# Kernel tuning notes

Measured on AMD Instinct MI355X. Metric: run time of the kernel, lower is better.

Reference implementation:

```python
import jax, jax.numpy as jnp
import numpy as np

NH = 12   # num_heads
EPS = 1e-6


def _layer_norm(x):
    m = jnp.mean(x, axis=-1, keepdims=True)
    v = jnp.mean((x - m) ** 2, axis=-1, keepdims=True)
    return (x - m) * jax.lax.rsqrt(v + EPS)


def _rms_norm(x, w):
    return x * jax.lax.rsqrt(jnp.mean(x * x, axis=-1, keepdims=True) + EPS) * w


def _rope_cos_sin(f, h, w, head_dim):
    # matches rope_params + calculate_freqs_i: split c=head_dim//2 complex freqs
    # into [c-2*(c//3), c//3, c//3] for the (F,H,W) axes.
    c = head_dim // 2
    inv = 1.0 / (10000.0 ** (np.arange(0, head_dim, 2, dtype=np.float64) / head_dim))
    c1 = c - 2 * (c // 3); c2 = c // 3
    af = np.outer(np.arange(f), inv[:c1])
    ah = np.outer(np.arange(h), inv[c1:c1 + c2])
    aw = np.outer(np.arange(w), inv[c1 + c2:])
    ang = np.concatenate([
        np.broadcast_to(af[:, None, None, :], (f, h, w, c1)),
        np.broadcast_to(ah[None, :, None, :], (f, h, w, c2)),
        np.broadcast_to(aw[None, None, :, :], (f, h, w, c2)),
    ], axis=-1).reshape(f * h * w, c)
    return jnp.asarray(np.cos(ang), jnp.float32), jnp.asarray(np.sin(ang), jnp.float32)


def _apply_rope(x, cos, sin):
    # complex rotation on interleaved pairs; x: [B,L,n,d]
    B, L, n, d = x.shape
    xr = x.reshape(B, L, n, d // 2, 2)
    x0, x1 = xr[..., 0], xr[..., 1]
    co = cos[None, :, None, :]; si = sin[None, :, None, :]
    return jnp.stack([x0 * co - x1 * si, x0 * si + x1 * co], axis=-1).reshape(B, L, n, d)


def _attention(q, k, v):
    scale = 1.0 / jnp.sqrt(jnp.asarray(q.shape[-1], q.dtype))
    s = jnp.einsum('blnd,bmnd->bnlm', q, k) * scale
    return jnp.einsum('bnlm,bmnd->blnd', jax.nn.softmax(s, axis=-1), v)


def _block(x, e, context, mod, sa_wq, sa_bq, sa_wk, sa_bk, sa_wv, sa_bv, sa_wo, sa_bo,
           sa_nq, sa_nk, n3_w, n3_b, ca_wq, ca_bq, ca_wk, ca_bk, ca_wv, ca_bv, ca_wo,
           ca_bo, ca_nq, ca_nk, ffn_w1, ffn_b1, ffn_w2, ffn_b2, f, h, w):
    B, L, C = x.shape
    D = C // NH
    em = mod + e                      # [B,6,C] AdaLN shift/scale/gate params
    cos, sin = _rope_cos_sin(f, h, w, D)
    # --- self-attention with AdaLN modulation + RoPE + qk RMSNorm ---
    xa = _layer_norm(x) * (1.0 + em[:, 1:2]) + em[:, 0:1]
    q = _rms_norm(xa @ sa_wq + sa_bq, sa_nq).reshape(B, L, NH, D)
    k = _rms_norm(xa @ sa_wk + sa_bk, sa_nk).reshape(B, L, NH, D)
    v = (xa @ sa_wv + sa_bv).reshape(B, L, NH, D)
    q = _apply_rope(q, cos, sin)
    k = _apply_rope(k, cos, sin)
    y = _attention(q, k, v).reshape(B, L, C) @ sa_wo + sa_bo
    x = x + y * em[:, 2:3]
    # --- t2v cross-attention (norm3 is affine LayerNorm) ---
    L2 = context.shape[1]
    xc = _layer_norm(x) * n3_w + n3_b
    q = _rms_norm(xc @ ca_wq + ca_bq, ca_nq).reshape(B, L, NH, D)
    k = _rms_norm(context @ ca_wk + ca_bk, ca_nk).reshape(B, L2, NH, D)
    v = (context @ ca_wv + ca_bv).reshape(B, L2, NH, D)
    x = x + (_attention(q, k, v).reshape(B, L, C) @ ca_wo + ca_bo)
    # --- FFN (GELU-tanh) with AdaLN modulation ---
    xf = _layer_norm(x) * (1.0 + em[:, 4:5]) + em[:, 3:4]
    y = jax.nn.gelu(xf @ ffn_w1 + ffn_b1, approximate=True) @ ffn_w2 + ffn_b2
    return x + y * em[:, 5:6]


def setup_inputs() -> dict:
    key = jax.random.key(0)
    ks = jax.random.split(key, 16)
    B, L2, C, FFN = 1, 512, 1536, 8960
    F, H, W = 9, 16, 28
    L = F * H * W  # 4032
    def mk(i, shape, s=0.02):
        return jax.random.normal(ks[i], shape, jnp.float32) * s
    return {
        'x': jax.random.normal(ks[0], (B, L, C), jnp.float32),
        'e': jax.random.normal(ks[1], (B, 6, C), jnp.float32),
        'context': jax.random.normal(ks[2], (B, L2, C), jnp.float32),
        'mod': jax.random.normal(ks[3], (1, 6, C), jnp.float32) / jnp.sqrt(float(C)),
        'sa_wq': mk(4, (C, C)), 'sa_bq': jnp.zeros((C,), jnp.float32),
        'sa_wk': mk(5, (C, C)), 'sa_bk': jnp.zeros((C,), jnp.float32),
        'sa_wv': mk(6, (C, C)), 'sa_bv': jnp.zeros((C,), jnp.float32),
        'sa_wo': mk(7, (C, C)), 'sa_bo': jnp.zeros((C,), jnp.float32),
        'sa_nq': jnp.ones((C,), jnp.float32), 'sa_nk': jnp.ones((C,), jnp.float32),
        'n3_w': jnp.ones((C,), jnp.float32), 'n3_b': jnp.zeros((C,), jnp.float32),
        'ca_wq': mk(8, (C, C)), 'ca_bq': jnp.zeros((C,), jnp.float32),
        'ca_wk': mk(9, (C, C)), 'ca_bk': jnp.zeros((C,), jnp.float32),
        'ca_wv': mk(10, (C, C)), 'ca_bv': jnp.zeros((C,), jnp.float32),
        'ca_wo': mk(11, (C, C)), 'ca_bo': jnp.zeros((C,), jnp.float32),
        'ca_nq': jnp.ones((C,), jnp.float32), 'ca_nk': jnp.ones((C,), jnp.float32),
        'ffn_w1': mk(12, (C, FFN)), 'ffn_b1': jnp.zeros((FFN,), jnp.float32),
        'ffn_w2': mk(13, (FFN, C)), 'ffn_b2': jnp.zeros((C,), jnp.float32),
        'f': F, 'h': H, 'w': W,
    }


def reference(x, e, context, mod, sa_wq, sa_bq, sa_wk, sa_bk, sa_wv, sa_bv, sa_wo,
              sa_bo, sa_nq, sa_nk, n3_w, n3_b, ca_wq, ca_bq, ca_wk, ca_bk, ca_wv,
              ca_bv, ca_wo, ca_bo, ca_nq, ca_nk, ffn_w1, ffn_b1, ffn_w2, ffn_b2,
              f, h, w):
    return _block(x, e, context, mod, sa_wq, sa_bq, sa_wk, sa_bk, sa_wv, sa_bv,
                  sa_wo, sa_bo, sa_nq, sa_nk, n3_w, n3_b, ca_wq, ca_bq, ca_wk,
                  ca_bk, ca_wv, ca_bv, ca_wo, ca_bo, ca_nq, ca_nk, ffn_w1, ffn_b1,
                  ffn_w2, ffn_b2, f, h, w)
```

## Files before the change

### kernel.cpp

```cpp
#include <hip/hip_runtime.h>
#include <math.h>


#define L_SEQ 4032
#define L_PAD 4096
#define C_DIM 1536
#define L_CTX 512
#define FFN_DIM 8960
#define NHEAD 12
#define DHEAD 128

typedef __attribute__((ext_vector_type(8))) short short8;
typedef __attribute__((ext_vector_type(4))) float floatx4;

__device__ inline unsigned short f2bf(float x) {
  unsigned int u = __float_as_uint(x);
  u += 0x7fffu + ((u >> 16) & 1u);
  return (unsigned short)(u >> 16);
}

__device__ inline float2 block_sum2(float2 v) {
  __shared__ float2 red[4];
#pragma unroll
  for (int o = 32; o > 0; o >>= 1) {
    v.x += __shfl_xor(v.x, o, 64);
    v.y += __shfl_xor(v.y, o, 64);
  }
  int wave = threadIdx.x >> 6;
  if ((threadIdx.x & 63) == 0) red[wave] = v;
  __syncthreads();
  float2 t = make_float2(0.f, 0.f);
#pragma unroll
  for (int i = 0; i < 4; ++i) { t.x += red[i].x; t.y += red[i].y; }
  return t;
}

__global__ void add_kernel(float* __restrict__ o, const float* __restrict__ a,
                           const float* __restrict__ b, int n) {
  int i = blockIdx.x * 256 + threadIdx.x;
  if (i < n) o[i] = a[i] + b[i];
}

__global__ void concat3_kernel(float* __restrict__ o, const float* __restrict__ a,
                               const float* __restrict__ b, const float* __restrict__ c) {
  int i = blockIdx.x * 256 + threadIdx.x;
  if (i < C_DIM) {
    o[i] = a[i];
    o[C_DIM + i] = b[i];
    if (c) o[2 * C_DIM + i] = c[i];
  }
}

__global__ void f32_to_bf16_kernel(unsigned short* __restrict__ o,
                                   const float* __restrict__ in, int n) {
  int i = (blockIdx.x * 256 + threadIdx.x) * 4;
  if (i < n) {
    float4 v = *(const float4*)&in[i];
    ushort4 o4 = {f2bf(v.x), f2bf(v.y), f2bf(v.z), f2bf(v.w)};
    *(ushort4*)&o[i] = o4;
  }
}

__global__ __launch_bounds__(256) void transpose_bf16_kernel(
    const float* __restrict__ W, unsigned short* __restrict__ WT, int K, int N) {
  __shared__ float t[32][33];
  int n0 = blockIdx.x * 32, k0 = blockIdx.y * 32;
  int c = threadIdx.x & 31, r0 = threadIdx.x >> 5;
#pragma unroll
  for (int i = 0; i < 4; ++i) {
    int r = r0 + 8 * i;
    t[r][c] = W[(size_t)(k0 + r) * N + n0 + c];
  }
  __syncthreads();
#pragma unroll
  for (int i = 0; i < 4; ++i) {
    int r = r0 + 8 * i;
    WT[(size_t)(n0 + r) * K + k0 + c] = f2bf(t[c][r]);
  }
}

__global__ __launch_bounds__(256) void transpose_v_kernel(
    const float* __restrict__ V, unsigned short* __restrict__ Vt, int stride, int Lk) {
  __shared__ float t[32][33];
  int k0 = blockIdx.x * 32, c0 = blockIdx.y * 32;
  int c = threadIdx.x & 31, r0 = threadIdx.x >> 5;
#pragma unroll
  for (int i = 0; i < 4; ++i) {
    int r = r0 + 8 * i;
    t[r][c] = V[(size_t)(k0 + r) * stride + c0 + c];
  }
  __syncthreads();
#pragma unroll
  for (int i = 0; i < 4; ++i) {
    int r = r0 + 8 * i;
    Vt[(size_t)(c0 + r) * Lk + k0 + c] = f2bf(t[c][r]);
  }
}

__global__ __launch_bounds__(256) void ln_affine_kernel(
    unsigned short* __restrict__ out, const float* __restrict__ in,
    const float* __restrict__ sc, const float* __restrict__ sh, float addOne) {
  int row = blockIdx.x;
  const float* xr = in + (size_t)row * C_DIM;
  float vals[C_DIM / 256];
  float2 p = make_float2(0.f, 0.f);
  int cnt = 0;
  for (int c = threadIdx.x; c < C_DIM; c += 256) {
    float v = xr[c];
    vals[cnt++] = v;
    p.x += v; p.y += v * v;
  }
  float2 t = block_sum2(p);
  float mean = t.x * (1.f / C_DIM);
  float var = t.y * (1.f / C_DIM) - mean * mean;
  float r = rsqrtf(var + 1e-6f);
  cnt = 0;
  for (int c = threadIdx.x; c < C_DIM; c += 256) {
    float xh = (vals[cnt++] - mean) * r;
    out[(size_t)row * C_DIM + c] = f2bf(xh * (addOne + sc[c]) + sh[c]);
  }
}

template <int ROPE>
__global__ __launch_bounds__(256) void rms_post_kernel(
    unsigned short* __restrict__ obf, const float* __restrict__ in,
    const float* __restrict__ w, const float* __restrict__ cosb,
    const float* __restrict__ sinb, int stride, float ps) {
  int row = blockIdx.x;
  const float* xr = in + (size_t)row * stride;
  int c0 = threadIdx.x * 6;
  float v[6];
  *(float2*)&v[0] = *(const float2*)&xr[c0];
  *(float2*)&v[2] = *(const float2*)&xr[c0 + 2];
  *(float2*)&v[4] = *(const float2*)&xr[c0 + 4];
  float s2 = 0.f;
#pragma unroll
  for (int i = 0; i < 6; ++i) s2 += v[i] * v[i];
  float2 t = block_sum2(make_float2(s2, 0.f));
  float r = rsqrtf(t.x * (1.f / C_DIM) + 1e-6f) * ps;
#pragma unroll
  for (int i = 0; i < 6; ++i) v[i] *= r * w[c0 + i];
  if (ROPE) {
#pragma unroll
    for (int i = 0; i < 3; ++i) {
      int c = c0 + 2 * i;
      int j = (c & 127) >> 1;
      float co = cosb[row * 64 + j], si = sinb[row * 64 + j];
      float a = v[2 * i], b = v[2 * i + 1];
      v[2 * i] = a * co - b * si;
      v[2 * i + 1] = a * si + b * co;
    }
  }
  unsigned short* op = obf + (size_t)row * C_DIM + c0;
  ushort2 o01 = {f2bf(v[0]), f2bf(v[1])};
  ushort2 o23 = {f2bf(v[2]), f2bf(v[3])};
  ushort2 o45 = {f2bf(v[4]), f2bf(v[5])};
  *(ushort2*)&op[0] = o01;
  *(ushort2*)&op[2] = o23;
  *(ushort2*)&op[4] = o45;
}

__global__ void rope_tables_kernel(float* __restrict__ cosb, float* __restrict__ sinb) {
  int l = blockIdx.x, j = threadIdx.x;
  int f = l / (16 * 28);
  int rem = l % (16 * 28);
  int hh = rem / 28, ww = rem % 28;
  double inv = pow(10000.0, -(double)(2 * j) / 128.0);
  double pos = (j < 22) ? (double)f : ((j < 43) ? (double)hh : (double)ww);
  double ang = pos * inv;
  cosb[l * 64 + j] = (float)cos(ang);
  sinb[l * 64 + j] = (float)sin(ang);
}

__device__ inline float gelu_tanh(float x) {
  float x3 = x * x * x;
  return 0.5f * x * (1.f + tanhf(0.79788456080286535588f * (x + 0.044715f * x3)));
}

__device__ inline int xcd_remap(int flat, int nwg) {
  int qq = nwg >> 3, rr = nwg & 7;
  int xcd = flat & 7, idx = flat >> 3;
  return (xcd < rr ? xcd * (qq + 1) : rr * (qq + 1) + (xcd - rr) * qq) + idx;
}

template <int EPI>
__global__ __launch_bounds__(256) void mgemm_kernel(
    const unsigned short* __restrict__ A, const unsigned short* __restrict__ BT,
    const float* __restrict__ bias, void* __restrict__ Cout,
    const float* __restrict__ resid, const float* __restrict__ gate,
    int N, int K, int Mlimit) {
  __shared__ short sA[3][4096];
  __shared__ short sB[3][4096];
  const int tid = threadIdx.x;
  const int wv = tid >> 6, lane = tid & 63;
  const int lm = lane & 15, lq = lane >> 4;
  const int wr = wv >> 1, wc = wv & 1;

  const int gx = gridDim.x;
  int flat = xcd_remap(blockIdx.y * gx + blockIdx.x, gx * gridDim.y);
  const int row0 = (flat / gx) * 128, col0 = (flat % gx) * 128;

  floatx4 zero4 = {0.f, 0.f, 0.f, 0.f};
  floatx4 acc[4][4];
#pragma unroll
  for (int i = 0; i < 4; ++i)
#pragma unroll
    for (int j = 0; j < 4; ++j) acc[i][j] = zero4;

  const unsigned short* Abase = A + ((size_t)row0 + lm) * K + lq * 8;
  const unsigned short* Bbase = BT + ((size_t)col0 + lm) * K + lq * 8;

  auto stage = [&](int buf, int k0) {
#pragma unroll
    for (int t = 0; t < 2; ++t) {
      int g = wv * 2 + t;
      __builtin_amdgcn_global_load_lds(
          (const __attribute__((address_space(1))) void*)(Abase + (size_t)(g * 16) * K + k0),
          (__attribute__((address_space(3))) void*)(sA[buf] + g * 512), 16, 0, 0);
      __builtin_amdgcn_global_load_lds(
          (const __attribute__((address_space(1))) void*)(Bbase + (size_t)(g * 16) * K + k0),
          (__attribute__((address_space(3))) void*)(sB[buf] + g * 512), 16, 0, 0);
    }
  };

  stage(0, 0);
  stage(1, 32);
  asm volatile("s_waitcnt vmcnt(4)" ::: "memory");
  __builtin_amdgcn_s_barrier();
  __builtin_amdgcn_sched_barrier(0);

  int cur = 0;
  const int nk = K >> 5;
  for (int t = 0; t < nk; ++t) {
    int b2 = cur + 2; if (b2 >= 3) b2 -= 3;
    const bool more = (t + 2 < nk);
    if (more) stage(b2, (t + 2) << 5);
    const short* sAc = &sA[cur][0];
    const short* sBc = &sB[cur][0];
    short8 af[4], bfv[4];
#pragma unroll
    for (int mt = 0; mt < 4; ++mt)
      af[mt] = *(const short8*)(sAc + (wr * 4 + mt) * 512 + lane * 8);
#pragma unroll
    for (int nt = 0; nt < 4; ++nt)
      bfv[nt] = *(const short8*)(sBc + (wc * 4 + nt) * 512 + lane * 8);
#pragma unroll
    for (int mt = 0; mt < 4; ++mt)
#pragma unroll
      for (int nt = 0; nt < 4; ++nt)
        acc[mt][nt] = __builtin_amdgcn_mfma_f32_16x16x32_bf16(
            af[mt], bfv[nt], acc[mt][nt], 0, 0, 0);
    __builtin_amdgcn_sched_barrier(0);
    if (more) { asm volatile("s_waitcnt vmcnt(4)" ::: "memory"); }
    else      { asm volatile("s_waitcnt vmcnt(0)" ::: "memory"); }
    __builtin_amdgcn_s_barrier();
    __builtin_amdgcn_sched_barrier(0);
    cur = (cur + 1 == 3) ? 0 : cur + 1;
  }

#pragma unroll
  for (int nt = 0; nt < 4; ++nt) {
    int colg = col0 + wc * 64 + nt * 16 + lm;
    float bv = bias[colg];
    float gv = (EPI == 2 && gate) ? gate[colg] : 1.f;
#pragma unroll
    for (int mt = 0; mt < 4; ++mt) {
#pragma unroll
      for (int r = 0; r < 4; ++r) {
        int rowg = row0 + wr * 64 + mt * 16 + lq * 4 + r;
        if (rowg < Mlimit) {
          float v = acc[mt][nt][r] + bv;
          if (EPI == 1) {
            ((unsigned short*)Cout)[(size_t)rowg * N + colg] = f2bf(gelu_tanh(v));
          } else if (EPI == 2) {
            ((float*)Cout)[(size_t)rowg * N + colg] =
                resid[(size_t)rowg * N + colg] + v * gv;
          } else {
            ((float*)Cout)[(size_t)rowg * N + colg] = v;
          }
        }
      }
    }
  }
}

template <int EPI>
__global__ __launch_bounds__(256) void mgemm64_kernel(
    const unsigned short* __restrict__ A, const unsigned short* __restrict__ BT,
    const float* __restrict__ bias, void* __restrict__ Cout,
    const float* __restrict__ resid, const float* __restrict__ gate,
    int N, int K, int Mlimit) {
  __shared__ short sA[3][2048];
  __shared__ short sB[3][4096];
  const int tid = threadIdx.x;
  const int wv = tid >> 6, lane = tid & 63;
  const int lm = lane & 15, lq = lane >> 4;
  const int wc = wv;

  const int gx = gridDim.x;
  int flat = xcd_remap(blockIdx.y * gx + blockIdx.x, gx * gridDim.y);
  const int row0 = (flat / gx) * 64, col0 = (flat % gx) * 128;

  floatx4 zero4 = {0.f, 0.f, 0.f, 0.f};
  floatx4 acc[4][2];
#pragma unroll
  for (int i = 0; i < 4; ++i)
#pragma unroll
    for (int j = 0; j < 2; ++j) acc[i][j] = zero4;

  const unsigned short* Abase = A + ((size_t)row0 + lm) * K + lq * 8;
  const unsigned short* Bbase = BT + ((size_t)col0 + lm) * K + lq * 8;

  auto stage = [&](int buf, int k0) {
    __builtin_amdgcn_global_load_lds(
        (const __attribute__((address_space(1))) void*)(Abase + (size_t)(wv * 16) * K + k0),
        (__attribute__((address_space(3))) void*)(sA[buf] + wv * 512), 16, 0, 0);
#pragma unroll
    for (int t = 0; t < 2; ++t) {
      int g = wv * 2 + t;
      __builtin_amdgcn_global_load_lds(
          (const __attribute__((address_space(1))) void*)(Bbase + (size_t)(g * 16) * K + k0),
          (__attribute__((address_space(3))) void*)(sB[buf] + g * 512), 16, 0, 0);
    }
  };

  stage(0, 0);
  stage(1, 32);
  asm volatile("s_waitcnt vmcnt(3)" ::: "memory");
  __builtin_amdgcn_s_barrier();
  __builtin_amdgcn_sched_barrier(0);

  int cur = 0;
  const int nk = K >> 5;
  for (int t = 0; t < nk; ++t) {
    int b2 = cur + 2; if (b2 >= 3) b2 -= 3;
    const bool more = (t + 2 < nk);
    if (more) stage(b2, (t + 2) << 5);
    const short* sAc = &sA[cur][0];
    const short* sBc = &sB[cur][0];
    short8 af[4], bfv[2];
#pragma unroll
    for (int mt = 0; mt < 4; ++mt)
      af[mt] = *(const short8*)(sAc + mt * 512 + lane * 8);
#pragma unroll
    for (int nt = 0; nt < 2; ++nt)
      bfv[nt] = *(const short8*)(sBc + (wc * 2 + nt) * 512 + lane * 8);
#pragma unroll
    for (int mt = 0; mt < 4; ++mt)
#pragma unroll
      for (int nt = 0; nt < 2; ++nt)
        acc[mt][nt] = __builtin_amdgcn_mfma_f32_16x16x32_bf16(
            af[mt], bfv[nt], acc[mt][nt], 0, 0, 0);
    __builtin_amdgcn_sched_barrier(0);
    if (more) { asm volatile("s_waitcnt vmcnt(3)" ::: "memory"); }
    else      { asm volatile("s_waitcnt vmcnt(0)" ::: "memory"); }
    __builtin_amdgcn_s_barrier();
    __builtin_amdgcn_sched_barrier(0);
    cur = (cur + 1 == 3) ? 0 : cur + 1;
  }

#pragma unroll
  for (int nt = 0; nt < 2; ++nt) {
    int colg = col0 + wc * 32 + nt * 16 + lm;
    float bv = bias[colg];
    float gv = (EPI == 2 && gate) ? gate[colg] : 1.f;
#pragma unroll
    for (int mt = 0; mt < 4; ++mt) {
#pragma unroll
      for (int r = 0; r < 4; ++r) {
        int rowg = row0 + mt * 16 + lq * 4 + r;
        if (rowg < Mlimit) {
          float v = acc[mt][nt][r] + bv;
          if (EPI == 1) {
            ((unsigned short*)Cout)[(size_t)rowg * N + colg] = f2bf(gelu_tanh(v));
          } else if (EPI == 2) {
            ((float*)Cout)[(size_t)rowg * N + colg] =
                resid[(size_t)rowg * N + colg] + v * gv;
          } else {
            ((float*)Cout)[(size_t)rowg * N + colg] = v;
          }
        }
      }
    }
  }
}

__global__ __launch_bounds__(256) void attn_mfma_kernel(
    const unsigned short* __restrict__ Qb, const unsigned short* __restrict__ Kb,
    const unsigned short* __restrict__ Vt, unsigned short* __restrict__ O,
    int Lk) {
  __shared__ short sK[2][4096];
  __shared__ short sV[2][4096];
  __shared__ short sP[4][512];
  const int h = blockIdx.y;
  const int q0 = blockIdx.x * 64;
  const int tid = threadIdx.x;
  const int wv = tid >> 6, lane = tid & 63;
  const int lm = lane & 15, lq = lane >> 4;

  short8 qf[4];
  {
    const unsigned short* qrow =
        Qb + (size_t)(q0 + wv * 16 + lm) * C_DIM + h * DHEAD + lq * 8;
#pragma unroll
    for (int dc = 0; dc < 4; ++dc) qf[dc] = *(const short8*)(qrow + dc * 32);
  }

  floatx4 zero4 = {0.f, 0.f, 0.f, 0.f};
  floatx4 acc[8];
#pragma unroll
  for (int g = 0; g < 8; ++g) acc[g] = zero4;
  float m = -1e30f, l = 0.f;

  auto stageKV = [&](int buf, int k0) {
#pragma unroll
    for (int t = 0; t < 2; ++t) {
      int g = wv * 2 + t;
      int nt_ = g >> 2, dc = g & 3;
      const unsigned short* srck =
          Kb + (size_t)(k0 + nt_ * 16 + lm) * C_DIM + h * DHEAD + dc * 32 + lq * 8;
      __builtin_amdgcn_global_load_lds(
          (const __attribute__((address_space(1))) void*)srck,
          (__attribute__((address_space(3))) void*)(sK[buf] + g * 512), 16, 0, 0);
      const unsigned short* srcv =
          Vt + (size_t)(h * DHEAD + g * 16 + lm) * Lk + k0 + lq * 8;
      __builtin_amdgcn_global_load_lds(
          (const __attribute__((address_space(1))) void*)srcv,
          (__attribute__((address_space(3))) void*)(sV[buf] + g * 512), 16, 0, 0);
    }
  };

  stageKV(0, 0);
  __syncthreads();
  int cur = 0;
  const int nsteps = Lk >> 5;
  for (int t = 0; t < nsteps; ++t) {
    if (t + 1 < nsteps) stageKV(cur ^ 1, (t + 1) << 5);
    const short* sKc = &sK[cur][0];
    const short* sVc = &sV[cur][0];

    floatx4 s0 = zero4, s1 = zero4;
#pragma unroll
    for (int dc = 0; dc < 4; ++dc) {
      short8 kf0 = *(const short8*)(sKc + dc * 512 + lane * 8);
      short8 kf1 = *(const short8*)(sKc + (4 + dc) * 512 + lane * 8);
      s0 = __builtin_amdgcn_mfma_f32_16x16x32_bf16(kf0, qf[dc], s0, 0, 0, 0);
      s1 = __builtin_amdgcn_mfma_f32_16x16x32_bf16(kf1, qf[dc], s1, 0, 0, 0);
    }

    float mx = fmaxf(fmaxf(fmaxf(s0[0], s0[1]), fmaxf(s0[2], s0[3])),
                     fmaxf(fmaxf(s1[0], s1[1]), fmaxf(s1[2], s1[3])));
    mx = fmaxf(mx, __shfl_xor(mx, 16));
    mx = fmaxf(mx, __shfl_xor(mx, 32));
    bool need = mx > m + 11.5f;
    if (__any((int)need)) {
      float mn = fmaxf(m, mx);
      float al = exp2f(m - mn);
      m = mn;
      l *= al;
      float ar[4];
#pragma unroll
      for (int r = 0; r < 4; ++r) ar[r] = __shfl(al, lq * 4 + r);
#pragma unroll
      for (int g = 0; g < 8; ++g)
#pragma unroll
        for (int r = 0; r < 4; ++r) acc[g][r] *= ar[r];
    }
    float rs = 0.f;
    ushort4 pk0, pk1;
#pragma unroll
    for (int r = 0; r < 4; ++r) {
      float p = exp2f(s0[r] - m);
      rs += p;
      ((unsigned short*)&pk0)[r] = f2bf(p);
    }
#pragma unroll
    for (int r = 0; r < 4; ++r) {
      float p = exp2f(s1[r] - m);
      rs += p;
      ((unsigned short*)&pk1)[r] = f2bf(p);
    }
    rs += __shfl_xor(rs, 16);
    rs += __shfl_xor(rs, 32);
    l += rs;
    {
      int baseq = (((lq >> 1) * 16 + lm) << 3) + ((lq & 1) << 2);
      *(ushort4*)&sP[wv][baseq] = pk0;
      *(ushort4*)&sP[wv][baseq + 256] = pk1;
    }
    asm volatile("" ::: "memory");
    short8 pa = *(const short8*)(&sP[wv][lane * 8]);
#pragma unroll
    for (int g = 0; g < 8; ++g) {
      short8 vf = *(const short8*)(sVc + g * 512 + lane * 8);
      acc[g] = __builtin_amdgcn_mfma_f32_16x16x32_bf16(pa, vf, acc[g], 0, 0, 0);
    }
    __syncthreads();
    cur ^= 1;
  }

  float invl[4];
#pragma unroll
  for (int r = 0; r < 4; ++r) invl[r] = 1.f / __shfl(l, lq * 4 + r);
  unsigned short* orow =
      O + (size_t)(q0 + wv * 16 + lq * 4) * C_DIM + h * DHEAD + lm;
#pragma unroll
  for (int g = 0; g < 8; ++g) {
#pragma unroll
    for (int r = 0; r < 4; ++r) {
      orow[(size_t)r * C_DIM + g * 16] = f2bf(acc[g][r] * invl[r]);
    }
  }
}

extern "C" void kernel_launch(void* const* d_in, const int* in_sizes, int n_in,
                              void* d_out, int out_size, void* d_ws, size_t ws_size,
                              hipStream_t stream) {
  const float* x     = (const float*)d_in[0];
  const float* e     = (const float*)d_in[1];
  const float* ctx   = (const float*)d_in[2];
  const float* mod   = (const float*)d_in[3];
  const float* sa_wq = (const float*)d_in[4];
  const float* sa_bq = (const float*)d_in[5];
  const float* sa_wk = (const float*)d_in[6];
  const float* sa_bk = (const float*)d_in[7];
  const float* sa_wv = (const float*)d_in[8];
  const float* sa_bv = (const float*)d_in[9];
  const float* sa_wo = (const float*)d_in[10];
  const float* sa_bo = (const float*)d_in[11];
  const float* sa_nq = (const float*)d_in[12];
  const float* sa_nk = (const float*)d_in[13];
  const float* n3_w  = (const float*)d_in[14];
  const float* n3_b  = (const float*)d_in[15];
  const float* ca_wq = (const float*)d_in[16];
  const float* ca_bq = (const float*)d_in[17];
  const float* ca_wk = (const float*)d_in[18];
  const float* ca_bk = (const float*)d_in[19];
  const float* ca_wv = (const float*)d_in[20];
  const float* ca_bv = (const float*)d_in[21];
  const float* ca_wo = (const float*)d_in[22];
  const float* ca_bo = (const float*)d_in[23];
  const float* ca_nq = (const float*)d_in[24];
  const float* ca_nk = (const float*)d_in[25];
  const float* ffn_w1 = (const float*)d_in[26];
  const float* ffn_b1 = (const float*)d_in[27];
  const float* ffn_w2 = (const float*)d_in[28];
  const float* ffn_b2 = (const float*)d_in[29];
  float* out = (float*)d_out;

  char* wsb = (char*)d_ws;
  auto alloc_f = [&](size_t n) { float* p = (float*)wsb; wsb += ((n * 4 + 255) / 256) * 256; return p; };
  auto alloc_h = [&](size_t n) { unsigned short* p = (unsigned short*)wsb; wsb += ((n * 2 + 255) / 256) * 256; return p; };

  float* em   = alloc_f(6 * C_DIM);
  float* cosb = alloc_f(L_SEQ * 64);
  float* sinb = alloc_f(L_SEQ * 64);
  float* qkv  = alloc_f((size_t)L_SEQ * 3 * C_DIM);
  float* x1b  = alloc_f((size_t)L_SEQ * C_DIM);
  unsigned short* act_bf  = alloc_h((size_t)L_PAD * C_DIM);
  unsigned short* ctx_bf  = alloc_h((size_t)L_CTX * C_DIM);
  unsigned short* wtqkv = alloc_h((size_t)3 * C_DIM * C_DIM);
  unsigned short* wto   = alloc_h((size_t)C_DIM * C_DIM);
  unsigned short* wtcq  = alloc_h((size_t)C_DIM * C_DIM);
  unsigned short* wtckv = alloc_h((size_t)2 * C_DIM * C_DIM);
  unsigned short* wtco  = alloc_h((size_t)C_DIM * C_DIM);
  unsigned short* wt1   = alloc_h((size_t)FFN_DIM * C_DIM);
  unsigned short* wt2   = alloc_h((size_t)C_DIM * FFN_DIM);
  float* qkv_bias = alloc_f(3 * C_DIM);
  float* ckv_bias = alloc_f(2 * C_DIM);
  unsigned short* kbf_x = alloc_h((size_t)L_CTX * C_DIM);
  unsigned short* vtx   = alloc_h((size_t)C_DIM * L_CTX);

  unsigned short* qbf_self = (unsigned short*)x1b;
  unsigned short* kbf_self = ((unsigned short*)x1b) + (size_t)L_SEQ * C_DIM;
  unsigned short* vt_self  = (unsigned short*)out;
  unsigned short* qbf_x    = (unsigned short*)out;
  float* crossq = qkv;
  float* ckv    = qkv + (size_t)L_SEQ * C_DIM;
  unsigned short* ffnh_bf = (unsigned short*)qkv;

  const float qscale = 0.12751649737103347f;

  dim3 gT(C_DIM / 32, C_DIM / 32);
  dim3 gQKV(3 * C_DIM / 128, L_PAD / 128);
  dim3 gGL64(C_DIM / 128, L_PAD / 64);
  dim3 gCKV64(2 * C_DIM / 128, L_CTX / 64);
  dim3 gAtt(L_SEQ / 64, NHEAD);

  transpose_bf16_kernel<<<gT, 256, 0, stream>>>(sa_wq, wtqkv, C_DIM, C_DIM);
  transpose_bf16_kernel<<<gT, 256, 0, stream>>>(sa_wk, wtqkv + (size_t)C_DIM * C_DIM, C_DIM, C_DIM);
  transpose_bf16_kernel<<<gT, 256, 0, stream>>>(sa_wv, wtqkv + (size_t)2 * C_DIM * C_DIM, C_DIM, C_DIM);
  transpose_bf16_kernel<<<gT, 256, 0, stream>>>(sa_wo, wto, C_DIM, C_DIM);
  transpose_bf16_kernel<<<gT, 256, 0, stream>>>(ca_wq, wtcq, C_DIM, C_DIM);
  transpose_bf16_kernel<<<gT, 256, 0, stream>>>(ca_wk, wtckv, C_DIM, C_DIM);
  transpose_bf16_kernel<<<gT, 256, 0, stream>>>(ca_wv, wtckv + (size_t)C_DIM * C_DIM, C_DIM, C_DIM);
  transpose_bf16_kernel<<<gT, 256, 0, stream>>>(ca_wo, wtco, C_DIM, C_DIM);
  transpose_bf16_kernel<<<dim3(FFN_DIM / 32, C_DIM / 32), 256, 0, stream>>>(ffn_w1, wt1, C_DIM, FFN_DIM);
  transpose_bf16_kernel<<<dim3(C_DIM / 32, FFN_DIM / 32), 256, 0, stream>>>(ffn_w2, wt2, FFN_DIM, C_DIM);
  f32_to_bf16_kernel<<<(L_CTX * C_DIM) / 1024, 256, 0, stream>>>(ctx_bf, ctx, L_CTX * C_DIM);
  concat3_kernel<<<6, 256, 0, stream>>>(qkv_bias, sa_bq, sa_bk, sa_bv);
  concat3_kernel<<<6, 256, 0, stream>>>(ckv_bias, ca_bk, ca_bv, nullptr);

  add_kernel<<<(6 * C_DIM + 255) / 256, 256, 0, stream>>>(em, e, mod, 6 * C_DIM);
  rope_tables_kernel<<<L_SEQ, 64, 0, stream>>>(cosb, sinb);

  ln_affine_kernel<<<L_SEQ, 256, 0, stream>>>(act_bf, x, em + C_DIM, em, 1.f);
  mgemm_kernel<0><<<gQKV, 256, 0, stream>>>(act_bf, wtqkv, qkv_bias, qkv,
                                            nullptr, nullptr, 3 * C_DIM, C_DIM, L_SEQ);
  rms_post_kernel<1><<<L_SEQ, 256, 0, stream>>>(qbf_self, qkv, sa_nq, cosb, sinb,
                                                3 * C_DIM, qscale);
  rms_post_kernel<1><<<L_SEQ, 256, 0, stream>>>(kbf_self, qkv + C_DIM, sa_nk, cosb, sinb,
                                                3 * C_DIM, 1.f);
  transpose_v_kernel<<<dim3(L_SEQ / 32, C_DIM / 32), 256, 0, stream>>>(
      qkv + 2 * C_DIM, vt_self, 3 * C_DIM, L_SEQ);
  attn_mfma_kernel<<<gAtt, 256, 0, stream>>>(qbf_self, kbf_self, vt_self, act_bf, L_SEQ);
  mgemm64_kernel<2><<<gGL64, 256, 0, stream>>>(act_bf, wto, sa_bo, x1b,
                                               x, em + 2 * C_DIM, C_DIM, C_DIM, L_SEQ);

  ln_affine_kernel<<<L_SEQ, 256, 0, stream>>>(act_bf, x1b, n3_w, n3_b, 0.f);
  mgemm64_kernel<0><<<gGL64, 256, 0, stream>>>(act_bf, wtcq, ca_bq, crossq,
                                               nullptr, nullptr, C_DIM, C_DIM, L_SEQ);
  rms_post_kernel<0><<<L_SEQ, 256, 0, stream>>>(qbf_x, crossq, ca_nq, cosb, sinb,
                                                C_DIM, qscale);
  mgemm64_kernel<0><<<gCKV64, 256, 0, stream>>>(ctx_bf, wtckv, ckv_bias, ckv,
                                                nullptr, nullptr, 2 * C_DIM, C_DIM, L_CTX);
  rms_post_kernel<0><<<L_CTX, 256, 0, stream>>>(kbf_x, ckv, ca_nk, cosb, sinb,
                                                2 * C_DIM, 1.f);
  transpose_v_kernel<<<dim3(L_CTX / 32, C_DIM / 32), 256, 0, stream>>>(
      ckv + C_DIM, vtx, 2 * C_DIM, L_CTX);
  attn_mfma_kernel<<<gAtt, 256, 0, stream>>>(qbf_x, kbf_x, vtx, act_bf, L_CTX);
  mgemm64_kernel<2><<<gGL64, 256, 0, stream>>>(act_bf, wtco, ca_bo, out,
                                               x1b, nullptr, C_DIM, C_DIM, L_SEQ);

  ln_affine_kernel<<<L_SEQ, 256, 0, stream>>>(act_bf, out, em + 4 * C_DIM, em + 3 * C_DIM, 1.f);
  dim3 g1(FFN_DIM / 128, L_PAD / 128);
  mgemm_kernel<1><<<g1, 256, 0, stream>>>(act_bf, wt1, ffn_b1, ffnh_bf,
                                          nullptr, nullptr, FFN_DIM, C_DIM, L_SEQ);
  dim3 g2(C_DIM / 128, L_PAD / 64);
  mgemm64_kernel<2><<<g2, 256, 0, stream>>>(ffnh_bf, wt2, ffn_b2, out,
                                            out, em + 5 * C_DIM, C_DIM, FFN_DIM, L_SEQ);
}
```

Measured before the change: 1.577 ms.

## Add 128x128 K=64 GEMM for FFN down-projection and triple-buffer attention KV

Adds a new GEMM kernel with 128x128 output tiles and a 64-wide K step, double-buffered in LDS, and uses it for the FFN second projection (K=8960) in place of the 64-row tile kernel. This halves the number of blocks and barriers per K element and increases A/B reuse. Separately, the attention kernel's K/V staging moves from two to three LDS buffers with a prefetch distance of two and partial vmcnt waits, so loads overlap more compute. The costs are more LDS per block, which may lower occupancy, and a grid of only 384 blocks for the down-projection, which may underfill the GPU.

```diff
diff --git a/kernel.cpp b/kernel.cpp
--- a/kernel.cpp
+++ b/kernel.cpp
@@ -285,6 +285,109 @@
 }
 
 template <int EPI>
+__global__ __launch_bounds__(256) void mgemm_k64_kernel(
+    const unsigned short* __restrict__ A, const unsigned short* __restrict__ BT,
+    const float* __restrict__ bias, void* __restrict__ Cout,
+    const float* __restrict__ resid, const float* __restrict__ gate,
+    int N, int K, int Mlimit) {
+  __shared__ short sA[2][8192];
+  __shared__ short sB[2][8192];
+  const int tid = threadIdx.x;
+  const int wv = tid >> 6, lane = tid & 63;
+  const int lm = lane & 15, lq = lane >> 4;
+  const int wr = wv >> 1, wc = wv & 1;
+
+  const int gx = gridDim.x;
+  int flat = xcd_remap(blockIdx.y * gx + blockIdx.x, gx * gridDim.y);
+  const int row0 = (flat / gx) * 128, col0 = (flat % gx) * 128;
+
+  floatx4 zero4 = {0.f, 0.f, 0.f, 0.f};
+  floatx4 acc[4][4];
+#pragma unroll
+  for (int i = 0; i < 4; ++i)
+#pragma unroll
+    for (int j = 0; j < 4; ++j) acc[i][j] = zero4;
+
+  const unsigned short* Abase = A + ((size_t)row0 + lm) * K + lq * 8;
+  const unsigned short* Bbase = BT + ((size_t)col0 + lm) * K + lq * 8;
+
+  auto stage = [&](int buf, int k0) {
+#pragma unroll
+    for (int kk = 0; kk < 2; ++kk) {
+#pragma unroll
+      for (int t = 0; t < 2; ++t) {
+        int g = wv * 2 + t;
+        __builtin_amdgcn_global_load_lds(
+            (const __attribute__((address_space(1))) void*)(Abase + (size_t)(g * 16) * K + k0 + kk * 32),
+            (__attribute__((address_space(3))) void*)(sA[buf] + kk * 4096 + g * 512), 16, 0, 0);
+        __builtin_amdgcn_global_load_lds(
+            (const __attribute__((address_space(1))) void*)(Bbase + (size_t)(g * 16) * K + k0 + kk * 32),
+            (__attribute__((address_space(3))) void*)(sB[buf] + kk * 4096 + g * 512), 16, 0, 0);
+      }
+    }
+  };
+
+  stage(0, 0);
+  asm volatile("s_waitcnt vmcnt(0)" ::: "memory");
+  __builtin_amdgcn_s_barrier();
+  __builtin_amdgcn_sched_barrier(0);
+
+  int cur = 0;
+  const int nk = K >> 6;
+  for (int t = 0; t < nk; ++t) {
+    if (t + 1 < nk) stage(cur ^ 1, (t + 1) << 6);
+#pragma unroll
+    for (int kk = 0; kk < 2; ++kk) {
+      const short* sAc = &sA[cur][kk * 4096];
+      const short* sBc = &sB[cur][kk * 4096];
+      short8 af[4], bfv[4];
+#pragma unroll
+      for (int mt = 0; mt < 4; ++mt)
+        af[mt] = *(const short8*)(sAc + (wr * 4 + mt) * 512 + lane * 8);
+#pragma unroll
+      for (int nt = 0; nt < 4; ++nt)
+        bfv[nt] = *(const short8*)(sBc + (wc * 4 + nt) * 512 + lane * 8);
+#pragma unroll
+      for (int mt = 0; mt < 4; ++mt)
+#pragma unroll
+        for (int nt = 0; nt < 4; ++nt)
+          acc[mt][nt] = __builtin_amdgcn_mfma_f32_16x16x32_bf16(
+              af[mt], bfv[nt], acc[mt][nt], 0, 0, 0);
+    }
+    __builtin_amdgcn_sched_barrier(0);
+    asm volatile("s_waitcnt vmcnt(0)" ::: "memory");
+    __builtin_amdgcn_s_barrier();
+    __builtin_amdgcn_sched_barrier(0);
+    cur ^= 1;
+  }
+
+#pragma unroll
+  for (int nt = 0; nt < 4; ++nt) {
+    int colg = col0 + wc * 64 + nt * 16 + lm;
+    float bv = bias[colg];
+    float gv = (EPI == 2 && gate) ? gate[colg] : 1.f;
+#pragma unroll
+    for (int mt = 0; mt < 4; ++mt) {
+#pragma unroll
+      for (int r = 0; r < 4; ++r) {
+        int rowg = row0 + wr * 64 + mt * 16 + lq * 4 + r;
+        if (rowg < Mlimit) {
+          float v = acc[mt][nt][r] + bv;
+          if (EPI == 1) {
+            ((unsigned short*)Cout)[(size_t)rowg * N + colg] = f2bf(gelu_tanh(v));
+          } else if (EPI == 2) {
+            ((float*)Cout)[(size_t)rowg * N + colg] =
+                resid[(size_t)rowg * N + colg] + v * gv;
+          } else {
+            ((float*)Cout)[(size_t)rowg * N + colg] = v;
+          }
+        }
+      }
+    }
+  }
+}
+
+template <int EPI>
 __global__ __launch_bounds__(256) void mgemm64_kernel(
     const unsigned short* __restrict__ A, const unsigned short* __restrict__ BT,
     const float* __restrict__ bias, void* __restrict__ Cout,
@@ -389,8 +492,8 @@
     const unsigned short* __restrict__ Qb, const unsigned short* __restrict__ Kb,
     const unsigned short* __restrict__ Vt, unsigned short* __restrict__ O,
     int Lk) {
-  __shared__ short sK[2][4096];
-  __shared__ short sV[2][4096];
+  __shared__ short sK[3][4096];
+  __shared__ short sV[3][4096];
   __shared__ short sP[4][512];
   const int h = blockIdx.y;
   const int q0 = blockIdx.x * 64;
@@ -431,11 +534,17 @@
   };
 
   stageKV(0, 0);
-  __syncthreads();
+  stageKV(1, 32);
+  asm volatile("s_waitcnt vmcnt(4)" ::: "memory");
+  __builtin_amdgcn_s_barrier();
+  __builtin_amdgcn_sched_barrier(0);
+
   int cur = 0;
   const int nsteps = Lk >> 5;
   for (int t = 0; t < nsteps; ++t) {
-    if (t + 1 < nsteps) stageKV(cur ^ 1, (t + 1) << 5);
+    int b2 = cur + 2; if (b2 >= 3) b2 -= 3;
+    const bool more = (t + 2 < nsteps);
+    if (more) stageKV(b2, (t + 2) << 5);
     const short* sKc = &sK[cur][0];
     const short* sVc = &sV[cur][0];
 
@@ -495,8 +604,12 @@
       short8 vf = *(const short8*)(sVc + g * 512 + lane * 8);
       acc[g] = __builtin_amdgcn_mfma_f32_16x16x32_bf16(pa, vf, acc[g], 0, 0, 0);
     }
-    __syncthreads();
-    cur ^= 1;
+    __builtin_amdgcn_sched_barrier(0);
+    if (more) { asm volatile("s_waitcnt vmcnt(4)" ::: "memory"); }
+    else      { asm volatile("s_waitcnt vmcnt(0)" ::: "memory"); }
+    __builtin_amdgcn_s_barrier();
+    __builtin_amdgcn_sched_barrier(0);
+    cur = (cur + 1 == 3) ? 0 : cur + 1;
   }
 
   float invl[4];
@@ -636,7 +749,7 @@
   dim3 g1(FFN_DIM / 128, L_PAD / 128);
   mgemm_kernel<1><<<g1, 256, 0, stream>>>(act_bf, wt1, ffn_b1, ffnh_bf,
                                           nullptr, nullptr, FFN_DIM, C_DIM, L_SEQ);
-  dim3 g2(C_DIM / 128, L_PAD / 64);
-  mgemm64_kernel<2><<<g2, 256, 0, stream>>>(ffnh_bf, wt2, ffn_b2, out,
-                                            out, em + 5 * C_DIM, C_DIM, FFN_DIM, L_SEQ);
-}
+  dim3 g2(C_DIM / 128, L_PAD / 128);
+  mgemm_k64_kernel<2><<<g2, 256, 0, stream>>>(ffnh_bf, wt2, ffn_b2, out,
+                                              out, em + 5 * C_DIM, C_DIM, FFN_DIM, L_SEQ);
+}
```

Result: faster. 1.530 ms (-3.0%).
